# Optimization experiments

Measured on AMD Instinct MI355X. Metric: run time of the kernel, lower is better.

Reference implementation:

```python
import jax, jax.numpy as jnp
import numpy as np

B, Lc, Le, H, V = 128, 512, 512, 512, 128
PAD_IDX = 0  # ignore_index for cross entropy


def _lstm_cell(x, h, c, Wih, Whh, bih, bhh):
    # PyTorch gate order: i, f, g, o
    gates = x @ Wih.T + h @ Whh.T + bih + bhh
    i, f, g, o = jnp.split(gates, 4, axis=-1)
    c_new = jax.nn.sigmoid(f) * c + jax.nn.sigmoid(i) * jnp.tanh(g)
    h_new = jax.nn.sigmoid(o) * jnp.tanh(c_new)
    return h_new, c_new


def setup_inputs() -> dict:
    key = jax.random.key(0)
    ks = jax.random.split(key, 16)
    s = 0.05  # weight init scale
    inp = {
        "C": jax.random.normal(ks[0], (B, Lc, V), jnp.float32),
        "C_pad": jax.random.randint(ks[1], (B, Lc), 0, 2, jnp.int32).at[:, 0].set(0),
        "E": jax.random.randint(ks[2], (B, Le), 0, V, jnp.int32),
        "E_emb": jax.random.normal(ks[3], (B, Le, V), jnp.float32),
        # encoder LSTM (input V -> hidden H)
        "enc_Wih": s * jax.random.normal(ks[4], (4 * H, V), jnp.float32),
        "enc_Whh": s * jax.random.normal(ks[5], (4 * H, H), jnp.float32),
        "enc_bih": jnp.zeros((4 * H,), jnp.float32),
        "enc_bhh": jnp.zeros((4 * H,), jnp.float32),
        # decoder LSTMCell (input V+H -> hidden H); input is concat([E_emb_t, V_prev])
        "dec_Wih": s * jax.random.normal(ks[6], (4 * H, V + H), jnp.float32),
        "dec_Whh": s * jax.random.normal(ks[7], (4 * H, H), jnp.float32),
        "dec_bih": jnp.zeros((4 * H,), jnp.float32),
        "dec_bhh": jnp.zeros((4 * H,), jnp.float32),
        # attention_proj: Linear(H, H, bias=False)
        "att_W": s * jax.random.normal(ks[8], (H, H), jnp.float32),
        # output_proj: Linear(2H, H)
        "out_W": s * jax.random.normal(ks[9], (H, 2 * H), jnp.float32),
        "out_b": jnp.zeros((H,), jnp.float32),
        # vocab_proj: Linear(H, V)
        "voc_W": s * jax.random.normal(ks[10], (V, H), jnp.float32),
        "voc_b": jnp.zeros((V,), jnp.float32),
    }
    return inp


def reference(C, C_pad, E, E_emb, enc_Wih, enc_Whh, enc_bih, enc_bhh,
              dec_Wih, dec_Whh, dec_bih, dec_bhh, att_W, out_W, out_b,
              voc_W, voc_b):
    Bv = C.shape[0]
    Hh = enc_Whh.shape[1]

    # ---- encoder LSTM over compressed input ----
    def enc_step(carry, x_t):
        h, c = carry
        h, c = _lstm_cell(x_t, h, c, enc_Wih, enc_Whh, enc_bih, enc_bhh)
        return (h, c), h

    h0 = jnp.zeros((Bv, Hh), C.dtype)
    (hT, cT), enc_hs = jax.lax.scan(enc_step, (h0, h0), jnp.swapaxes(C, 0, 1))
    enc_hs = jnp.swapaxes(enc_hs, 0, 1)  # (B, Lc, H)
    pad = C_pad.astype(bool)              # (B, Lc)

    # ---- decoder loop (training mode, teacher forcing) ----
    def dec_step(carry, e_t):
        h, c, Vprev = carry
        x = jnp.concatenate([e_t, Vprev], axis=1)  # (B, V+H)
        h, c = _lstm_cell(x, h, c, dec_Wih, dec_Whh, dec_bih, dec_bhh)
        q = h @ att_W.T                                    # (B, H)
        scores = jnp.einsum('blh,bh->bl', enc_hs, q)       # (B, Lc)
        scores = jnp.where(pad, -jnp.inf, scores)
        d = jax.nn.softmax(scores, axis=1)
        attn = jnp.einsum('bl,blh->bh', d, enc_hs)         # (B, H)
        U = jnp.concatenate([h, attn], axis=1)             # (B, 2H)
        Vnew = U @ out_W.T + out_b                         # (B, H)
        # dropout treated as identity (eval-mode determinism)
        logits = jnp.tanh(Vnew) @ voc_W.T + voc_b          # (B, V)
        return (h, c, Vnew), logits

    Vinit = jnp.zeros((Bv, Hh), C.dtype)
    _, logits = jax.lax.scan(dec_step, (hT, cT, Vinit),
                             jnp.swapaxes(E_emb[:, :-1], 0, 1))
    logits = jnp.swapaxes(logits, 0, 1)  # (B, Le-1, V)

    # ---- cross entropy with ignore_index=PAD_IDX ----
    targets = E[:, 1:].astype(jnp.int32)
    logp = jax.nn.log_softmax(logits, axis=-1)
    nll = -jnp.take_along_axis(logp, targets[..., None], axis=-1)[..., 0]
    mask = (targets != PAD_IDX).astype(nll.dtype)
    loss = jnp.sum(nll * mask) / jnp.maximum(jnp.sum(mask), 1.0)
    return loss
```

## Files before the change

kernel.cpp:

```cpp
#include <hip/hip_runtime.h>
#include <hip/hip_bf16.h>


#define NWG 256
#define NT  256

typedef unsigned short u16;
typedef unsigned int   u32;
typedef unsigned long long u64;
typedef __attribute__((ext_vector_type(4))) float f4;
typedef __attribute__((ext_vector_type(8))) short s8;

constexpr int Bv = 128, Lc = 512, Le = 512, Hd = 512, Vc = 128;
constexpr int KE = 640;
constexpr int KD = 1152;

constexpr size_t O_WENC = 4096;
constexpr size_t O_WDEC = O_WENC + (size_t)2048*KE*2;
constexpr size_t O_ATTW = O_WDEC + (size_t)2048*KD*2;
constexpr size_t O_OUTW = O_ATTW + (size_t)512*512*2;
constexpr size_t O_VOCW = O_OUTW + (size_t)512*1024*2;
constexpr size_t O_BE   = O_VOCW + (size_t)128*512*2;
constexpr size_t O_BD   = O_BE + 8192;
constexpr size_t O_H    = O_BD + 8192;
constexpr size_t O_VPRV = O_H + (size_t)2*128*512*2;
constexpr size_t O_Q    = O_VPRV + (size_t)128*512*2;
constexpr size_t O_TNH  = O_Q + (size_t)128*512*4;
constexpr size_t O_PFX  = O_TNH + (size_t)2*128*512*2;
constexpr size_t O_CNT  = O_PFX + (size_t)128*512*4;
constexpr size_t O_PMS  = O_CNT + 512;
constexpr size_t O_PACC = O_PMS + 2048;
constexpr size_t O_LOSS = O_PACC + (size_t)256*512*2;
constexpr size_t O_ENC  = O_LOSS + 256;

constexpr int SM_U     = 64*KD*2;
constexpr int SM_BYTES = SM_U + 16384;

struct P {
  const float *C; const int *Cpad; const int *E; const float *Eemb;
  const float *eWih,*eWhh,*ebih,*ebhh;
  const float *dWih,*dWhh,*dbih,*dbhh;
  const float *attW,*outW,*outb,*vocW,*vocb;
  char* ws; float* out;
};

__device__ inline u16 f2bf(float x){
  u32 u = __float_as_uint(x);
  return (u16)((u + 0x7fffu + ((u>>16)&1u)) >> 16);
}
__device__ inline float bf2f(u16 b){ return __uint_as_float(((u32)b)<<16); }
__device__ inline float sigm(float x){ return 1.f/(1.f+expf(-x)); }

__device__ inline f4 MM(s8 a, s8 b, f4 c){
  return __builtin_amdgcn_mfma_f32_16x16x32_bf16(a, b, c, 0, 0, 0);
}

__device__ inline u64 ld64a(const void* p){
  return __hip_atomic_load((const u64*)p, __ATOMIC_RELAXED, __HIP_MEMORY_SCOPE_AGENT);
}
__device__ inline u32 ld32u(const void* p){
  return __hip_atomic_load((const u32*)p, __ATOMIC_RELAXED, __HIP_MEMORY_SCOPE_AGENT);
}
__device__ inline void st64a(void* p, u64 v){
  __hip_atomic_store((u64*)p, v, __ATOMIC_RELAXED, __HIP_MEMORY_SCOPE_AGENT);
}
__device__ inline void st32a(void* p, u32 v){
  __hip_atomic_store((u32*)p, v, __ATOMIC_RELAXED, __HIP_MEMORY_SCOPE_AGENT);
}
__device__ inline s8 ld16a(const void* p){
  union { u64 q[2]; s8 v; } u;
  u.q[0] = ld64a(p);
  u.q[1] = ld64a((const char*)p + 8);
  return u.v;
}

__device__ inline s8 cvt8(const float* p){
  f4 u = *(const f4*)p, v = *(const f4*)(p+4);
  s8 r;
  r[0]=(short)f2bf(u[0]); r[1]=(short)f2bf(u[1]); r[2]=(short)f2bf(u[2]); r[3]=(short)f2bf(u[3]);
  r[4]=(short)f2bf(v[0]); r[5]=(short)f2bf(v[1]); r[6]=(short)f2bf(v[2]); r[7]=(short)f2bf(v[3]);
  return r;
}

__device__ inline s8 ldsB(const char* sm, int K, int srow, int k){
  int byte = srow*(K*2) + k*2;
  byte ^= (srow&7)<<4;
  return *(const s8*)(sm + byte);
}

__device__ inline float wredmax(float v){
  #pragma unroll
  for (int m=32;m;m>>=1) v = fmaxf(v, __shfl_xor(v,m,64));
  return v;
}
__device__ inline float wredsum(float v){
  #pragma unroll
  for (int m=32;m;m>>=1) v += __shfl_xor(v,m,64);
  return v;
}

extern "C" __global__ void __launch_bounds__(NT,1) k_main(P p)
{
  extern __shared__ char sm[];
  const int wg = blockIdx.x, tid = threadIdx.x;
  const int gt = wg*NT + tid;
  const int rg = wg & 7, cg = wg >> 3;
  const int lid = rg*32 + cg;

  char* ws = p.ws;
  u32*  barAll  = (u32*)ws;
  u32*  flagAll = (u32*)(ws + 128);
  u32*  barRG   = (u32*)(ws + 512 + rg*256);
  u32*  flagRG  = (u32*)(ws + 512 + rg*256 + 128);
  u16*  wenc = (u16*)(ws + O_WENC);
  u16*  wdec = (u16*)(ws + O_WDEC);
  u16*  attw = (u16*)(ws + O_ATTW);
  u16*  outw = (u16*)(ws + O_OUTW);
  u16*  vocw = (u16*)(ws + O_VOCW);
  float* be  = (float*)(ws + O_BE);
  float* bd  = (float*)(ws + O_BD);
  u16*  hbf  = (u16*)(ws + O_H);
  u16*  vpv  = (u16*)(ws + O_VPRV);
  float* qg  = (float*)(ws + O_Q);
  u16*  tnhb = (u16*)(ws + O_TNH);
  u32*  pfx  = (u32*)(ws + O_PFX);
  u32*  cntp = (u32*)(ws + O_CNT);
  u64*  pms  = (u64*)(ws + O_PMS);
  u16*  pacc16 = (u16*)(ws + O_PACC);
  float* losp= (float*)(ws + O_LOSS);
  u16*  encc = (u16*)(ws + O_ENC);

  u32 genA = 0, genG = 0;

  auto GBall = [&](){
    genA++;
    __syncthreads();
    if (tid == 0){
      __builtin_amdgcn_fence(__ATOMIC_RELEASE, "agent");
      u32 old = __hip_atomic_fetch_add(barAll, 1u, __ATOMIC_RELAXED, __HIP_MEMORY_SCOPE_AGENT);
      if (old == genA*(u32)NWG - 1u) st32a(flagAll, genA);
      else while (ld32u(flagAll) < genA) __builtin_amdgcn_s_sleep(2);
      __builtin_amdgcn_fence(__ATOMIC_ACQUIRE, "agent");
    }
    __syncthreads();
  };
  auto RGB = [&](){
    genG++;
    __syncthreads();
    if (tid == 0){
      u32 old = __hip_atomic_fetch_add(barRG, 1u, __ATOMIC_RELAXED, __HIP_MEMORY_SCOPE_AGENT);
      if (old == genG*32u - 1u) st32a(flagRG, genG);
      else while (ld32u(flagRG) < genG) __builtin_amdgcn_s_sleep(2);
      __builtin_amdgcn_fence(__ATOMIC_ACQUIRE, "workgroup");
    }
    __syncthreads();
  };

  for (int i = gt; i < 2048*KE; i += NWG*NT){
    int row = i / KE, k = i - row*KE;
    float v = (k < 128) ? p.eWih[row*128 + k] : p.eWhh[row*512 + (k-128)];
    wenc[i] = f2bf(v);
  }
  for (int i = gt; i < 2048*KD; i += NWG*NT){
    int row = i / KD, k = i - row*KD;
    float v = (k < 640) ? p.dWih[row*640 + k] : p.dWhh[row*512 + (k-640)];
    wdec[i] = f2bf(v);
  }
  for (int i = gt; i < 512*512;  i += NWG*NT) attw[i] = f2bf(p.attW[i]);
  for (int i = gt; i < 512*1024; i += NWG*NT) outw[i] = f2bf(p.outW[i]);
  for (int i = gt; i < 128*512;  i += NWG*NT) vocw[i] = f2bf(p.vocW[i]);
  for (int i = gt; i < 2048;     i += NWG*NT){ be[i] = p.ebih[i]+p.ebhh[i]; bd[i] = p.dbih[i]+p.dbhh[i]; }
  { u32* hz = (u32*)hbf; for (int i = gt; i < 65536; i += NWG*NT) hz[i] = 0; }
  { u32* vz = (u32*)vpv; for (int i = gt; i < 32768; i += NWG*NT) vz[i] = 0; }
  if (gt == 0){ losp[0] = 0.f; losp[1] = 0.f; }
  if (wg < 128){
    int* padl = (int*)(sm + SM_U);
    for (int i = tid; i < 512; i += NT) padl[i] = p.Cpad[wg*512 + i];
    __syncthreads();
    if (tid == 0){
      u32 run = 0;
      for (int tt = 0; tt < 512; tt++){ pfx[wg*512+tt] = run; if (padl[tt] == 0) run++; }
      cntp[wg] = run;
    }
    __syncthreads();
  }
  GBall();

  const int l  = tid & 63, wv = tid >> 6;
  const int n2 = wv >> 1, k2 = wv & 1;
  const int kl = (l>>4) << 3;
  const int ar = rg*16 + (l&15);
  float cst = 0.f;
  float accN = 0.f, accC = 0.f;

  auto S6 = [&](int tl){
    const u16* tb = tnhb + (size_t)(tl&1)*Bv*Hd;
    float* lg = (float*)(sm + SM_U + 8192);
    s8 ta[16];
    #pragma unroll
    for (int ks = 0; ks < 16; ks++)
      ta[ks] = ld16a(tb + (size_t)(rg*16+(l&15))*Hd + ks*32 + kl);
    f4 lac0 = {0,0,0,0}, lac1 = {0,0,0,0};
    const int c0 = (wv*2)*16 + (l&15), c1 = (wv*2+1)*16 + (l&15);
    #pragma unroll
    for (int ks = 0; ks < 16; ks++){
      int k = ks*32 + kl;
      lac0 = MM(ta[ks], *(const s8*)(vocw + (size_t)c0*Hd + k), lac0);
      lac1 = MM(ta[ks], *(const s8*)(vocw + (size_t)c1*Hd + k), lac1);
    }
    #pragma unroll
    for (int r = 0; r < 4; r++){
      int row = ((l>>4)<<2) + r;
      lg[row*128 + c0] = lac0[r] + p.vocb[c0];
      lg[row*128 + c1] = lac1[r] + p.vocb[c1];
    }
    __syncthreads();
    {
      int rowi = tid>>4, ii = tid&15, b = rg*16 + rowi;
      float lm = -1e30f;
      #pragma unroll
      for (int j=0;j<8;j++) lm = fmaxf(lm, lg[rowi*128 + ii*8 + j]);
      #pragma unroll
      for (int m=1;m<16;m<<=1) lm = fmaxf(lm, __shfl_xor(lm,m,64));
      float le = 0.f;
      #pragma unroll
      for (int j=0;j<8;j++) le += expf(lg[rowi*128 + ii*8 + j] - lm);
      #pragma unroll
      for (int m=1;m<16;m<<=1) le += __shfl_xor(le,m,64);
      if (ii == 0){
        int tgt = p.E[b*Le + tl + 1];
        if (tgt != 0){ accN += logf(le) + lm - lg[rowi*128 + tgt]; accC += 1.f; }
      }
    }
    __syncthreads();
  };

  {
    const int chunks = KE/8;
    for (int idx = tid; idx < 64*chunks; idx += NT){
      int s = idx / chunks, cc = idx - s*chunks;
      int grow = (s>>4)*512 + cg*16 + (s&15);
      uint4 v = *(const uint4*)(wenc + (size_t)grow*KE + cc*8);
      int byte = s*(KE*2) + cc*16; byte ^= (s&7)<<4;
      *(uint4*)(sm + byte) = v;
    }
  }
  __syncthreads();

  for (int t = 0; t < Lc; t++){
    const u16* hold = hbf + (t&1)*Bv*Hd;
    u16* hnew       = hbf + ((t+1)&1)*Bv*Hd;
    s8 a[10];
    #pragma unroll
    for (int ks = 0; ks < 10; ks++){
      int k = k2*320 + ks*32 + kl;
      if (k < 128) a[ks] = cvt8(p.C + ((size_t)ar*Lc + t)*Vc + k);
      else         a[ks] = ld16a(hold + (size_t)ar*Hd + (k-128));
    }
    f4 acc0 = {0,0,0,0}, acc1 = {0,0,0,0};
    #pragma unroll
    for (int ks = 0; ks < 10; ks++){
      int k = k2*320 + ks*32 + kl;
      acc0 = MM(a[ks], ldsB(sm, KE, (n2*2+0)*16 + (l&15), k), acc0);
      acc1 = MM(a[ks], ldsB(sm, KE, (n2*2+1)*16 + (l&15), k), acc1);
    }
    float* exch = (float*)(sm + SM_U);
    #pragma unroll
    for (int r = 0; r < 4; r++){
      int row = ((l>>4)<<2) + r;
      exch[((k2*4 + n2*2+0)*16 + row)*16 + (l&15)] = acc0[r];
      exch[((k2*4 + n2*2+1)*16 + row)*16 + (l&15)] = acc1[r];
    }
    __syncthreads();
    {
      int row = tid >> 4, u = tid & 15;
      int gb = cg*16 + u;
      float gi = exch[((0)*16+row)*16+u] + exch[((4)*16+row)*16+u] + be[0*512+gb];
      float gf = exch[((1)*16+row)*16+u] + exch[((5)*16+row)*16+u] + be[1*512+gb];
      float gg = exch[((2)*16+row)*16+u] + exch[((6)*16+row)*16+u] + be[2*512+gb];
      float go = exch[((3)*16+row)*16+u] + exch[((7)*16+row)*16+u] + be[3*512+gb];
      float fi = sigm(gi), ff = sigm(gf), fg = tanhf(gg), fo = sigm(go);
      cst = ff*cst + fi*fg;
      float hn = fo * tanhf(cst);
      int b = rg*16 + row;
      u32 hb = f2bf(hn);
      u32 nb = __shfl_xor((int)hb, 1, 64);
      if ((tid & 1) == 0){
        u32 pk = hb | (nb << 16);
        st32a(hnew + (size_t)b*Hd + gb, pk);
        if (p.Cpad[b*Lc + t] == 0){
          u32 pos = pfx[b*Lc + t];
          st32a(encc + ((size_t)b*Lc + pos)*Hd + gb, pk);
        }
      }
    }
    RGB();
  }

  GBall();

  {
    const int chunks = KD/8;
    for (int idx = tid; idx < 64*chunks; idx += NT){
      int s = idx / chunks, cc = idx - s*chunks;
      int grow = (s>>4)*512 + cg*16 + (s&15);
      uint4 v = *(const uint4*)(wdec + (size_t)grow*KD + cc*8);
      int byte = s*(KD*2) + cc*16; byte ^= (s&7)<<4;
      *(uint4*)(sm + byte) = v;
    }
  }
  __syncthreads();

  for (int t = 0; t < Le-1; t++){
    const u16* hold = hbf + (t&1)*Bv*Hd;
    u16* hnew       = hbf + ((t+1)&1)*Bv*Hd;

    {
      s8 a[18];
      #pragma unroll
      for (int ks = 0; ks < 18; ks++){
        int k = k2*576 + ks*32 + kl;
        if (k < 128)      a[ks] = cvt8(p.Eemb + ((size_t)ar*Le + t)*Vc + k);
        else if (k < 640) a[ks] = ld16a(vpv  + (size_t)ar*Hd + (k-128));
        else              a[ks] = ld16a(hold + (size_t)ar*Hd + (k-640));
      }
      f4 acc0 = {0,0,0,0}, acc1 = {0,0,0,0};
      #pragma unroll
      for (int ks = 0; ks < 18; ks++){
        int k = k2*576 + ks*32 + kl;
        acc0 = MM(a[ks], ldsB(sm, KD, (n2*2+0)*16 + (l&15), k), acc0);
        acc1 = MM(a[ks], ldsB(sm, KD, (n2*2+1)*16 + (l&15), k), acc1);
      }
      float* exch = (float*)(sm + SM_U);
      #pragma unroll
      for (int r = 0; r < 4; r++){
        int row = ((l>>4)<<2) + r;
        exch[((k2*4 + n2*2+0)*16 + row)*16 + (l&15)] = acc0[r];
        exch[((k2*4 + n2*2+1)*16 + row)*16 + (l&15)] = acc1[r];
      }
      __syncthreads();
      {
        int row = tid >> 4, u = tid & 15;
        int gb = cg*16 + u;
        float gi = exch[((0)*16+row)*16+u] + exch[((4)*16+row)*16+u] + bd[0*512+gb];
        float gf = exch[((1)*16+row)*16+u] + exch[((5)*16+row)*16+u] + bd[1*512+gb];
        float gg = exch[((2)*16+row)*16+u] + exch[((6)*16+row)*16+u] + bd[2*512+gb];
        float go = exch[((3)*16+row)*16+u] + exch[((7)*16+row)*16+u] + bd[3*512+gb];
        float fi = sigm(gi), ff = sigm(gf), fg = tanhf(gg), fo = sigm(go);
        cst = ff*cst + fi*fg;
        float hn = fo * tanhf(cst);
        u32 hb = f2bf(hn);
        u32 nb = __shfl_xor((int)hb, 1, 64);
        if ((tid & 1) == 0)
          st32a(hnew + (size_t)(rg*16+row)*Hd + gb, hb | (nb << 16));
      }
    }
    RGB();

    {
      s8 ha[4];
      #pragma unroll
      for (int j = 0; j < 4; j++){
        int k = (wv*4 + j)*32 + kl;
        ha[j] = ld16a(hnew + (size_t)(rg*16 + (l&15))*Hd + k);
      }
      f4 acc = {0,0,0,0};
      #pragma unroll
      for (int j = 0; j < 4; j++){
        int k = (wv*4 + j)*32 + kl;
        acc = MM(ha[j], *(const s8*)(attw + (size_t)(cg*16 + (l&15))*Hd + k), acc);
      }
      float* exch4 = (float*)(sm + SM_U);
      #pragma unroll
      for (int r = 0; r < 4; r++)
        exch4[wv*256 + (((l>>4)<<2)+r)*16 + (l&15)] = acc[r];
      __syncthreads();
      {
        int row = tid >> 4, col = tid & 15;
        float q = exch4[row*16+col] + exch4[256+row*16+col]
                + exch4[512+row*16+col] + exch4[768+row*16+col];
        float qn = __shfl_xor(q, 1, 64);
        if ((tid & 1) == 0){
          union { u64 u; float f[2]; } pk; pk.f[0]=q; pk.f[1]=qn;
          st64a(qg + (size_t)(rg*16+row)*Hd + cg*16 + col, pk.u);
        }
      }
    }
    RGB();

    {
      const int row = rg*16 + (cg >> 1), hf = cg & 1;
      const int cn = (int)cntp[row], c2 = cn >> 1;
      const int st = hf ? c2 : 0, en = hf ? cn : c2, n = en - st;
      float* qld = (float*)(sm + SM_U);
      float* scl = (float*)(sm + SM_U + 2048);
      float* red = (float*)(sm + SM_U + 3104);
      float* part= (float*)(sm + SM_U + 8192);
      {
        union { u64 q; float f[2]; } u;
        u.q = ld64a(qg + (size_t)row*Hd + 2*tid);
        int c0 = 2*tid, c1 = c0+1;
        qld[(c0&15)*32 + (c0>>4)] = u.f[0];
        qld[(c1&15)*32 + (c1>>4)] = u.f[1];
      }
      __syncthreads();
      const int pg8 = tid >> 5, hg32 = tid & 31;
      const u16* ebase = encc + ((size_t)row*Lc + st)*Hd;
      for (int i = pg8; i < n; i += 8){
        const u16* e = ebase + (size_t)i*Hd + hg32*16;
        s8 ev0 = *(const s8*)(e);
        s8 ev1 = *(const s8*)(e+8);
        float s = 0.f;
        #pragma unroll
        for (int j=0;j<8;j++) s += bf2f((u16)ev0[j]) * qld[j*32+hg32];
        #pragma unroll
        for (int j=0;j<8;j++) s += bf2f((u16)ev1[j]) * qld[(j+8)*32+hg32];
        #pragma unroll
        for (int m=1;m<32;m<<=1) s += __shfl_xor(s, m, 64);
        if (hg32 == 0) scl[i] = s;
      }
      __syncthreads();
      float mloc = -1e30f;
      for (int i = tid; i < n; i += NT) mloc = fmaxf(mloc, scl[i]);
      mloc = wredmax(mloc);
      if ((tid&63)==0) red[tid>>6] = mloc;
      __syncthreads();
      float M = fmaxf(fmaxf(red[0],red[1]), fmaxf(red[2],red[3]));
      __syncthreads();
      float sloc = 0.f;
      for (int i = tid; i < n; i += NT){ float w = expf(scl[i]-M); scl[i]=w; sloc += w; }
      sloc = wredsum(sloc);
      if ((tid&63)==0) red[tid>>6] = sloc;
      __syncthreads();
      float S = red[0]+red[1]+red[2]+red[3];
      const int hg64 = tid & 63;
      float a8[8] = {0,0,0,0,0,0,0,0};
      const u16* eb2 = ebase + hg64*8;
      int i = wv;
      for (; i + 12 < n; i += 16){
        s8 e0 = *(const s8*)(eb2 + (size_t)i*Hd);
        s8 e1 = *(const s8*)(eb2 + (size_t)(i+4)*Hd);
        s8 e2 = *(const s8*)(eb2 + (size_t)(i+8)*Hd);
        s8 e3 = *(const s8*)(eb2 + (size_t)(i+12)*Hd);
        float w0=scl[i], w1=scl[i+4], w2=scl[i+8], w3=scl[i+12];
        #pragma unroll
        for (int j=0;j<8;j++) a8[j] += w0*bf2f((u16)e0[j]);
        #pragma unroll
        for (int j=0;j<8;j++) a8[j] += w1*bf2f((u16)e1[j]);
        #pragma unroll
        for (int j=0;j<8;j++) a8[j] += w2*bf2f((u16)e2[j]);
        #pragma unroll
        for (int j=0;j<8;j++) a8[j] += w3*bf2f((u16)e3[j]);
      }
      for (; i < n; i += 4){
        s8 e0 = *(const s8*)(eb2 + (size_t)i*Hd);
        float w0 = scl[i];
        #pragma unroll
        for (int j=0;j<8;j++) a8[j] += w0*bf2f((u16)e0[j]);
      }
      { f4 v0 = {a8[0],a8[1],a8[2],a8[3]}, v1 = {a8[4],a8[5],a8[6],a8[7]};
        *(f4*)(part + wv*512 + hg64*8)     = v0;
        *(f4*)(part + wv*512 + hg64*8 + 4) = v1; }
      __syncthreads();
      {
        int h0 = tid*2;
        float s0 = 0.f, s1 = 0.f;
        #pragma unroll
        for (int pg = 0; pg < 4; pg++){
          float2 pr = *(float2*)(part + pg*512 + h0);
          s0 += pr.x; s1 += pr.y;
        }
        u32 pk = (u32)f2bf(s0) | ((u32)f2bf(s1) << 16);
        st32a(pacc16 + (size_t)lid*Hd + h0, pk);
      }
      if (tid == 0){
        union { u64 q; float f[2]; } pk; pk.f[0]=M; pk.f[1]=S;
        st64a(pms + lid, pk.q);
      }
    }
    RGB();

    {
      float* sc2 = (float*)(sm + SM_U);
      float* vex = (float*)(sm + SM_U + 4096);
      if (tid < 16){
        union { u64 q; float f[2]; } uA, uB;
        uA.q = ld64a(pms + rg*32 + 2*tid);
        uB.q = ld64a(pms + rg*32 + 2*tid + 1);
        float M = fmaxf(uA.f[0], uB.f[0]);
        float eA = expf(uA.f[0]-M), eB = expf(uB.f[0]-M);
        float den = uA.f[1]*eA + uB.f[1]*eB;
        sc2[2*tid]   = eA/den;
        sc2[2*tid+1] = eB/den;
      }
      __syncthreads();
      if (cg == 0 && t > 0) S6(t-1);
      const int colc = cg*16 + (l&15);
      const u16* pb0 = pacc16 + ((size_t)(rg*32 + (l&15)*2))*Hd;
      float scA = sc2[(l&15)*2], scB = sc2[(l&15)*2+1];
      s8 raw[12];
      #pragma unroll
      for (int ks = 0; ks < 12; ks++){
        int km = wv*12 + ks;
        const void* ap;
        if (km < 16)      ap = hnew + (size_t)(rg*16+(l&15))*Hd + km*32 + kl;
        else if (km < 32) ap = pb0 + (km-16)*32 + kl;
        else              ap = pb0 + Hd + (km-32)*32 + kl;
        raw[ks] = ld16a(ap);
      }
      f4 vac = {0,0,0,0};
      #pragma unroll
      for (int ks = 0; ks < 12; ks++){
        int km = wv*12 + ks;
        s8 af;
        if (km < 16) af = raw[ks];
        else {
          float sc = (km < 32) ? scA : scB;
          #pragma unroll
          for (int j = 0; j < 8; j++) af[j] = (short)f2bf(bf2f((u16)raw[ks][j]) * sc);
        }
        int k = (km < 16) ? km*32+kl : ((km < 32) ? 512 + (km-16)*32+kl : 512 + (km-32)*32+kl);
        vac = MM(af, *(const s8*)(outw + (size_t)colc*1024 + k), vac);
      }
      #pragma unroll
      for (int r = 0; r < 4; r++)
        vex[wv*256 + (((l>>4)<<2)+r)*16 + (l&15)] = vac[r];
      __syncthreads();
      {
        int row = tid >> 4, col = tid & 15;
        float v = vex[row*16+col] + vex[256+row*16+col]
                + vex[512+row*16+col] + vex[768+row*16+col] + p.outb[cg*16+col];
        u32 vb = f2bf(v), tb2 = f2bf(tanhf(v));
        u32 vn = __shfl_xor((int)vb, 1, 64);
        u32 tn2 = __shfl_xor((int)tb2, 1, 64);
        if ((tid & 1) == 0){
          int b = rg*16 + row;
          u16* tnw = tnhb + (size_t)(t&1)*Bv*Hd;
          st32a(vpv + (size_t)b*Hd + cg*16 + col, vb | (vn<<16));
          st32a(tnw + (size_t)b*Hd + cg*16 + col, tb2 | (tn2<<16));
        }
      }
    }
    RGB();
  }

  if (cg == 0) S6(Le-2);

  if (cg == 0 && (tid&15) == 0){
    atomicAdd(losp + 0, accN);
    atomicAdd(losp + 1, accC);
  }
  GBall();
  if (wg == 0 && tid == 0) p.out[0] = losp[0] / fmaxf(losp[1], 1.f);
}

extern "C" void kernel_launch(void* const* d_in, const int* in_sizes, int n_in,
                              void* d_out, int out_size, void* d_ws, size_t ws_size,
                              hipStream_t stream)
{
  hipFuncSetAttribute(reinterpret_cast<const void*>(k_main),
                      hipFuncAttributeMaxDynamicSharedMemorySize, SM_BYTES);
  hipMemsetAsync(d_ws, 0, 4096, stream);

  P prm;
  prm.C    = (const float*)d_in[0];
  prm.Cpad = (const int*)  d_in[1];
  prm.E    = (const int*)  d_in[2];
  prm.Eemb = (const float*)d_in[3];
  prm.eWih = (const float*)d_in[4];
  prm.eWhh = (const float*)d_in[5];
  prm.ebih = (const float*)d_in[6];
  prm.ebhh = (const float*)d_in[7];
  prm.dWih = (const float*)d_in[8];
  prm.dWhh = (const float*)d_in[9];
  prm.dbih = (const float*)d_in[10];
  prm.dbhh = (const float*)d_in[11];
  prm.attW = (const float*)d_in[12];
  prm.outW = (const float*)d_in[13];
  prm.outb = (const float*)d_in[14];
  prm.vocW = (const float*)d_in[15];
  prm.vocb = (const float*)d_in[16];
  prm.ws   = (char*)d_ws;
  prm.out  = (float*)d_out;

  k_main<<<dim3(NWG), dim3(NT), SM_BYTES, stream>>>(prm);
}
```

Measured before the change: 26.10 ms.

## Fold output projection into decoder LSTM weights and cut per-step barriers

Precomputes fused decoder weights by multiplying the V_prev slice of dec_Wih by out_W, so the next step's gates come straight from h and the attention context rather than a materialised V. This removes one grid-group barrier phase per timestep. The step also merges the attention query, an online-softmax attention pass and a distributed vocab-projection cross-entropy that is combined one step later, and the group-barrier spin sleep is shortened. In exchange there is a heavy serial fp32 prefold at startup and a different bf16 rounding path, which may shift numerics.

Measured after the change: 35.73 ms. 1.37x slower.

```diff
diff --git a/kernel.cpp b/kernel.cpp
--- a/kernel.cpp
+++ b/kernel.cpp
@@ -11,26 +11,26 @@
 typedef __attribute__((ext_vector_type(4))) float f4;
 typedef __attribute__((ext_vector_type(8))) short s8;
 
-constexpr int Bv = 128, Lc = 512, Le = 512, Hd = 512, Vc = 128;
-constexpr int KE = 640;
-constexpr int KD = 1152;
+constexpr int Bv=128, Lc=512, Le=512, Hd=512, Vc=128;
+constexpr int KE=640, KD=1152;
 
 constexpr size_t O_WENC = 4096;
 constexpr size_t O_WDEC = O_WENC + (size_t)2048*KE*2;
-constexpr size_t O_ATTW = O_WDEC + (size_t)2048*KD*2;
+constexpr size_t O_WDF  = O_WDEC + (size_t)2048*KD*2;
+constexpr size_t O_ATTW = O_WDF  + (size_t)2048*KD*2;
 constexpr size_t O_OUTW = O_ATTW + (size_t)512*512*2;
 constexpr size_t O_VOCW = O_OUTW + (size_t)512*1024*2;
 constexpr size_t O_BE   = O_VOCW + (size_t)128*512*2;
 constexpr size_t O_BD   = O_BE + 8192;
-constexpr size_t O_H    = O_BD + 8192;
-constexpr size_t O_VPRV = O_H + (size_t)2*128*512*2;
-constexpr size_t O_Q    = O_VPRV + (size_t)128*512*2;
-constexpr size_t O_TNH  = O_Q + (size_t)128*512*4;
+constexpr size_t O_BDF  = O_BD + 8192;
+constexpr size_t O_H    = O_BDF + 8192;
+constexpr size_t O_TNH  = O_H + (size_t)2*128*512*2;
 constexpr size_t O_PFX  = O_TNH + (size_t)2*128*512*2;
 constexpr size_t O_CNT  = O_PFX + (size_t)128*512*4;
 constexpr size_t O_PMS  = O_CNT + 512;
 constexpr size_t O_PACC = O_PMS + 2048;
-constexpr size_t O_LOSS = O_PACC + (size_t)256*512*2;
+constexpr size_t O_REC  = O_PACC + (size_t)256*512*2;
+constexpr size_t O_LOSS = O_REC + (size_t)2*128*2*4*4;
 constexpr size_t O_ENC  = O_LOSS + 256;
 
 constexpr int SM_U     = 64*KD*2;
@@ -50,11 +50,9 @@
 }
 __device__ inline float bf2f(u16 b){ return __uint_as_float(((u32)b)<<16); }
 __device__ inline float sigm(float x){ return 1.f/(1.f+expf(-x)); }
-
 __device__ inline f4 MM(s8 a, s8 b, f4 c){
   return __builtin_amdgcn_mfma_f32_16x16x32_bf16(a, b, c, 0, 0, 0);
 }
-
 __device__ inline u64 ld64a(const void* p){
   return __hip_atomic_load((const u64*)p, __ATOMIC_RELAXED, __HIP_MEMORY_SCOPE_AGENT);
 }
@@ -69,11 +67,9 @@
 }
 __device__ inline s8 ld16a(const void* p){
   union { u64 q[2]; s8 v; } u;
-  u.q[0] = ld64a(p);
-  u.q[1] = ld64a((const char*)p + 8);
+  u.q[0] = ld64a(p); u.q[1] = ld64a((const char*)p + 8);
   return u.v;
 }
-
 __device__ inline s8 cvt8(const float* p){
   f4 u = *(const f4*)p, v = *(const f4*)(p+4);
   s8 r;
@@ -81,13 +77,11 @@
   r[4]=(short)f2bf(v[0]); r[5]=(short)f2bf(v[1]); r[6]=(short)f2bf(v[2]); r[7]=(short)f2bf(v[3]);
   return r;
 }
-
 __device__ inline s8 ldsB(const char* sm, int K, int srow, int k){
   int byte = srow*(K*2) + k*2;
   byte ^= (srow&7)<<4;
   return *(const s8*)(sm + byte);
 }
-
 __device__ inline float wredmax(float v){
   #pragma unroll
   for (int m=32;m;m>>=1) v = fmaxf(v, __shfl_xor(v,m,64));
@@ -97,6 +91,15 @@
   #pragma unroll
   for (int m=32;m;m>>=1) v += __shfl_xor(v,m,64);
   return v;
+}
+__device__ inline float dscore(s8 e, const float* q8){
+  float d = bf2f((u16)e[0])*q8[0] + bf2f((u16)e[1])*q8[1]
+          + bf2f((u16)e[2])*q8[2] + bf2f((u16)e[3])*q8[3]
+          + bf2f((u16)e[4])*q8[4] + bf2f((u16)e[5])*q8[5]
+          + bf2f((u16)e[6])*q8[6] + bf2f((u16)e[7])*q8[7];
+  #pragma unroll
+  for (int mk=1; mk<64; mk<<=1) d += __shfl_xor(d, mk, 64);
+  return d;
 }
 
 extern "C" __global__ void __launch_bounds__(NT,1) k_main(P p)
@@ -105,7 +108,6 @@
   const int wg = blockIdx.x, tid = threadIdx.x;
   const int gt = wg*NT + tid;
   const int rg = wg & 7, cg = wg >> 3;
-  const int lid = rg*32 + cg;
 
   char* ws = p.ws;
   u32*  barAll  = (u32*)ws;
@@ -114,24 +116,24 @@
   u32*  flagRG  = (u32*)(ws + 512 + rg*256 + 128);
   u16*  wenc = (u16*)(ws + O_WENC);
   u16*  wdec = (u16*)(ws + O_WDEC);
+  u16*  wdf  = (u16*)(ws + O_WDF);
   u16*  attw = (u16*)(ws + O_ATTW);
   u16*  outw = (u16*)(ws + O_OUTW);
   u16*  vocw = (u16*)(ws + O_VOCW);
   float* be  = (float*)(ws + O_BE);
   float* bd  = (float*)(ws + O_BD);
+  float* bdf = (float*)(ws + O_BDF);
   u16*  hbf  = (u16*)(ws + O_H);
-  u16*  vpv  = (u16*)(ws + O_VPRV);
-  float* qg  = (float*)(ws + O_Q);
   u16*  tnhb = (u16*)(ws + O_TNH);
   u32*  pfx  = (u32*)(ws + O_PFX);
   u32*  cntp = (u32*)(ws + O_CNT);
   u64*  pms  = (u64*)(ws + O_PMS);
   u16*  pacc16 = (u16*)(ws + O_PACC);
+  float* rec = (float*)(ws + O_REC);
   float* losp= (float*)(ws + O_LOSS);
   u16*  encc = (u16*)(ws + O_ENC);
 
   u32 genA = 0, genG = 0;
-
   auto GBall = [&](){
     genA++;
     __syncthreads();
@@ -150,7 +152,7 @@
     if (tid == 0){
       u32 old = __hip_atomic_fetch_add(barRG, 1u, __ATOMIC_RELAXED, __HIP_MEMORY_SCOPE_AGENT);
       if (old == genG*32u - 1u) st32a(flagRG, genG);
-      else while (ld32u(flagRG) < genG) __builtin_amdgcn_s_sleep(2);
+      else while (ld32u(flagRG) < genG) __builtin_amdgcn_s_sleep(1);
       __builtin_amdgcn_fence(__ATOMIC_ACQUIRE, "workgroup");
     }
     __syncthreads();
@@ -171,8 +173,51 @@
   for (int i = gt; i < 128*512;  i += NWG*NT) vocw[i] = f2bf(p.vocW[i]);
   for (int i = gt; i < 2048;     i += NWG*NT){ be[i] = p.ebih[i]+p.ebhh[i]; bd[i] = p.dbih[i]+p.dbhh[i]; }
   { u32* hz = (u32*)hbf; for (int i = gt; i < 65536; i += NWG*NT) hz[i] = 0; }
-  { u32* vz = (u32*)vpv; for (int i = gt; i < 32768; i += NWG*NT) vz[i] = 0; }
   if (gt == 0){ losp[0] = 0.f; losp[1] = 0.f; }
+
+  {
+    const int g0 = wg*8;
+    float* dv = (float*)sm;
+    for (int i = tid; i < 8*512; i += NT)
+      dv[i] = p.dWih[(size_t)(g0 + (i>>9))*640 + 128 + (i&511)];
+    __syncthreads();
+    float wa[8][4];
+    #pragma unroll
+    for (int r=0;r<8;r++){ wa[r][0]=0;wa[r][1]=0;wa[r][2]=0;wa[r][3]=0; }
+    for (int o = 0; o < 512; o++){
+      float b0 = p.outW[(size_t)o*1024 + tid];
+      float b1 = p.outW[(size_t)o*1024 + 256 + tid];
+      float b2 = p.outW[(size_t)o*1024 + 512 + tid];
+      float b3 = p.outW[(size_t)o*1024 + 768 + tid];
+      #pragma unroll
+      for (int r=0;r<8;r++){
+        float d = dv[r*512+o];
+        wa[r][0] += d*b0; wa[r][1] += d*b1; wa[r][2] += d*b2; wa[r][3] += d*b3;
+      }
+    }
+    #pragma unroll
+    for (int r=0;r<8;r++){
+      int g = g0 + r;
+      #pragma unroll
+      for (int j=0;j<4;j++){
+        int c = tid + 256*j;
+        if (c < 512) wdf[(size_t)g*KD + 128 + c] = f2bf(p.dWhh[(size_t)g*512 + c] + wa[r][j]);
+        else         wdf[(size_t)g*KD + 640 + (c-512)] = f2bf(wa[r][j]);
+      }
+    }
+    for (int i = tid; i < 8*128; i += NT){
+      int r = i >> 7, k = i & 127;
+      wdf[(size_t)(g0+r)*KD + k] = f2bf(p.dWih[(size_t)(g0+r)*640 + k]);
+    }
+    if (tid < 8){
+      int g = g0 + tid;
+      float s = p.dbih[g] + p.dbhh[g];
+      for (int o = 0; o < 512; o++) s += dv[tid*512+o]*p.outb[o];
+      bdf[g] = s;
+    }
+    __syncthreads();
+  }
+
   if (wg < 128){
     int* padl = (int*)(sm + SM_U);
     for (int i = tid; i < 512; i += NT) padl[i] = p.Cpad[wg*512 + i];
@@ -192,48 +237,6 @@
   const int ar = rg*16 + (l&15);
   float cst = 0.f;
   float accN = 0.f, accC = 0.f;
-
-  auto S6 = [&](int tl){
-    const u16* tb = tnhb + (size_t)(tl&1)*Bv*Hd;
-    float* lg = (float*)(sm + SM_U + 8192);
-    s8 ta[16];
-    #pragma unroll
-    for (int ks = 0; ks < 16; ks++)
-      ta[ks] = ld16a(tb + (size_t)(rg*16+(l&15))*Hd + ks*32 + kl);
-    f4 lac0 = {0,0,0,0}, lac1 = {0,0,0,0};
-    const int c0 = (wv*2)*16 + (l&15), c1 = (wv*2+1)*16 + (l&15);
-    #pragma unroll
-    for (int ks = 0; ks < 16; ks++){
-      int k = ks*32 + kl;
-      lac0 = MM(ta[ks], *(const s8*)(vocw + (size_t)c0*Hd + k), lac0);
-      lac1 = MM(ta[ks], *(const s8*)(vocw + (size_t)c1*Hd + k), lac1);
-    }
-    #pragma unroll
-    for (int r = 0; r < 4; r++){
-      int row = ((l>>4)<<2) + r;
-      lg[row*128 + c0] = lac0[r] + p.vocb[c0];
-      lg[row*128 + c1] = lac1[r] + p.vocb[c1];
-    }
-    __syncthreads();
-    {
-      int rowi = tid>>4, ii = tid&15, b = rg*16 + rowi;
-      float lm = -1e30f;
-      #pragma unroll
-      for (int j=0;j<8;j++) lm = fmaxf(lm, lg[rowi*128 + ii*8 + j]);
-      #pragma unroll
-      for (int m=1;m<16;m<<=1) lm = fmaxf(lm, __shfl_xor(lm,m,64));
-      float le = 0.f;
-      #pragma unroll
-      for (int j=0;j<8;j++) le += expf(lg[rowi*128 + ii*8 + j] - lm);
-      #pragma unroll
-      for (int m=1;m<16;m<<=1) le += __shfl_xor(le,m,64);
-      if (ii == 0){
-        int tgt = p.E[b*Le + tl + 1];
-        if (tgt != 0){ accN += logf(le) + lm - lg[rowi*128 + tgt]; accC += 1.f; }
-      }
-    }
-    __syncthreads();
-  };
 
   {
     const int chunks = KE/8;
@@ -304,34 +307,93 @@
     for (int idx = tid; idx < 64*chunks; idx += NT){
       int s = idx / chunks, cc = idx - s*chunks;
       int grow = (s>>4)*512 + cg*16 + (s&15);
-      uint4 v = *(const uint4*)(wdec + (size_t)grow*KD + cc*8);
+      uint4 v = *(const uint4*)(wdf + (size_t)grow*KD + cc*8);
       int byte = s*(KD*2) + cc*16; byte ^= (s&7)<<4;
       *(uint4*)(sm + byte) = v;
     }
   }
   __syncthreads();
+
+  float* exch = (float*)(sm + SM_U);
+  float* vex  = (float*)(sm + SM_U + 8192);
+  float* sc2  = (float*)(sm + SM_U + 12288);
+
+  auto CEREC = [&](int tl, int row, int half){
+    u32* th16 = (u32*)(sm + SM_U + 12416);
+    float* lgp = (float*)(sm + SM_U + 13440);
+    float* lgh = (float*)(sm + SM_U + 14464);
+    const u16* tb = tnhb + (size_t)(tl&1)*Bv*Hd + (size_t)row*Hd;
+    th16[tid & 255] = ld32u(tb + 2*tid);
+    __syncthreads();
+    {
+      int v = tid & 63, ksl = tid >> 6;
+      int gv = half*64 + v;
+      const u16* wp = vocw + (size_t)gv*Hd + ksl*128;
+      const u16* hp = (const u16*)th16 + ksl*128;
+      float acc = 0.f;
+      #pragma unroll 4
+      for (int j = 0; j < 16; j++){
+        s8 wv8 = *(const s8*)(wp + j*8);
+        #pragma unroll
+        for (int q = 0; q < 8; q++) acc += bf2f((u16)wv8[q]) * bf2f(hp[j*8+q]);
+      }
+      lgp[ksl*64 + v] = acc;
+    }
+    __syncthreads();
+    if (tid < 64){
+      int gv = half*64 + tid;
+      float lv = lgp[tid] + lgp[64+tid] + lgp[128+tid] + lgp[192+tid] + p.vocb[gv];
+      lgh[tid] = lv;
+      float m = wredmax(lv);
+      float s = wredsum(expf(lv - m));
+      if (tid == 0){
+        int tgt = p.E[row*Le + tl + 1];
+        float tlg = (tgt >= half*64 && tgt < half*64+64) ? lgh[tgt - half*64] : 0.f;
+        float* rp = rec + ((size_t)(tl&1)*256 + row*2 + half)*4;
+        union { u64 q; float f[2]; } pk; pk.f[0]=m; pk.f[1]=s;
+        st64a(rp, pk.q);
+        st32a(rp+2, __float_as_uint(tlg));
+      }
+    }
+    __syncthreads();
+  };
+  auto COMB = [&](int tl, int row){
+    int tgt = p.E[row*Le + tl + 1];
+    if (tgt != 0){
+      const float* rp = rec + ((size_t)(tl&1)*256 + row*2)*4;
+      union { u64 q; float f[2]; } a, b;
+      a.q = ld64a(rp); b.q = ld64a(rp+4);
+      float tA = __uint_as_float(ld32u(rp+2)), tB = __uint_as_float(ld32u(rp+6));
+      float M = fmaxf(a.f[0], b.f[0]);
+      float S = a.f[1]*expf(a.f[0]-M) + b.f[1]*expf(b.f[0]-M);
+      accN += logf(S) + M - (tA + tB);
+      accC += 1.f;
+    }
+  };
 
   for (int t = 0; t < Le-1; t++){
     const u16* hold = hbf + (t&1)*Bv*Hd;
     u16* hnew       = hbf + ((t+1)&1)*Bv*Hd;
 
-    {
-      s8 a[18];
-      #pragma unroll
-      for (int ks = 0; ks < 18; ks++){
-        int k = k2*576 + ks*32 + kl;
-        if (k < 128)      a[ks] = cvt8(p.Eemb + ((size_t)ar*Le + t)*Vc + k);
-        else if (k < 640) a[ks] = ld16a(vpv  + (size_t)ar*Hd + (k-128));
-        else              a[ks] = ld16a(hold + (size_t)ar*Hd + (k-640));
+    if (t == 0){
+      s8 a[10];
+      #pragma unroll
+      for (int ks = 0; ks < 10; ks++){
+        int ke = (k2==0) ? ((ks<4) ? ks*32+kl : 640 + (ks-4)*32 + kl)
+                         : (832 + ks*32 + kl);
+        if (ke < 128) a[ks] = cvt8(p.Eemb + ((size_t)ar*Le + 0)*Vc + ke);
+        else          a[ks] = ld16a(hold + (size_t)ar*Hd + (ke-640));
       }
       f4 acc0 = {0,0,0,0}, acc1 = {0,0,0,0};
       #pragma unroll
-      for (int ks = 0; ks < 18; ks++){
-        int k = k2*576 + ks*32 + kl;
-        acc0 = MM(a[ks], ldsB(sm, KD, (n2*2+0)*16 + (l&15), k), acc0);
-        acc1 = MM(a[ks], ldsB(sm, KD, (n2*2+1)*16 + (l&15), k), acc1);
-      }
-      float* exch = (float*)(sm + SM_U);
+      for (int ks = 0; ks < 10; ks++){
+        int ke = (k2==0) ? ((ks<4) ? ks*32+kl : 640 + (ks-4)*32 + kl)
+                         : (832 + ks*32 + kl);
+        int g0r = (n2*2+0)*512 + cg*16 + (l&15);
+        int g1r = (n2*2+1)*512 + cg*16 + (l&15);
+        acc0 = MM(a[ks], *(const s8*)(wdec + (size_t)g0r*KD + ke), acc0);
+        acc1 = MM(a[ks], *(const s8*)(wdec + (size_t)g1r*KD + ke), acc1);
+      }
       #pragma unroll
       for (int r = 0; r < 4; r++){
         int row = ((l>>4)<<2) + r;
@@ -352,203 +414,260 @@
         u32 hb = f2bf(hn);
         u32 nb = __shfl_xor((int)hb, 1, 64);
         if ((tid & 1) == 0)
-          st32a(hnew + (size_t)(rg*16+row)*Hd + gb, hb | (nb << 16));
-      }
-    }
-    RGB();
-
-    {
-      s8 ha[4];
-      #pragma unroll
-      for (int j = 0; j < 4; j++){
-        int k = (wv*4 + j)*32 + kl;
-        ha[j] = ld16a(hnew + (size_t)(rg*16 + (l&15))*Hd + k);
-      }
-      f4 acc = {0,0,0,0};
-      #pragma unroll
-      for (int j = 0; j < 4; j++){
-        int k = (wv*4 + j)*32 + kl;
-        acc = MM(ha[j], *(const s8*)(attw + (size_t)(cg*16 + (l&15))*Hd + k), acc);
-      }
-      float* exch4 = (float*)(sm + SM_U);
-      #pragma unroll
-      for (int r = 0; r < 4; r++)
-        exch4[wv*256 + (((l>>4)<<2)+r)*16 + (l&15)] = acc[r];
+          st32a(hnew + (size_t)(rg*16+(tid>>4))*Hd + gb, hb | (nb << 16));
+      }
+    } else {
+      if (tid < 16){
+        union { u64 q; float f[2]; } uA, uB;
+        uA.q = ld64a(pms + (rg*16+tid)*2 + 0);
+        uB.q = ld64a(pms + (rg*16+tid)*2 + 1);
+        float M = fmaxf(uA.f[0], uB.f[0]);
+        float eA = (uA.f[0] > -1e29f) ? expf(uA.f[0]-M) : 0.f;
+        float eB = (uB.f[0] > -1e29f) ? expf(uB.f[0]-M) : 0.f;
+        float den = uA.f[1]*eA + uB.f[1]*eB;
+        sc2[tid*2]   = eA/den;
+        sc2[tid*2+1] = eB/den;
+      }
+      __syncthreads();
+      const float scA = sc2[(l&15)*2], scB = sc2[(l&15)*2+1];
+      const u16* pA = pacc16 + (size_t)(ar*2+0)*Hd;
+      const u16* pB = pacc16 + (size_t)(ar*2+1)*Hd;
+      s8 a[18];
+      #pragma unroll
+      for (int ks = 0; ks < 18; ks++){
+        int k = k2*576 + ks*32 + kl;
+        if (k < 128)      a[ks] = cvt8(p.Eemb + ((size_t)ar*Le + t)*Vc + k);
+        else if (k < 640) a[ks] = ld16a(hold + (size_t)ar*Hd + (k-128));
+        else {
+          s8 va = ld16a(pA + (k-640));
+          s8 vb = ld16a(pB + (k-640));
+          s8 r;
+          #pragma unroll
+          for (int j = 0; j < 8; j++)
+            r[j] = (short)f2bf(scA*bf2f((u16)va[j]) + scB*bf2f((u16)vb[j]));
+          a[ks] = r;
+        }
+      }
+      f4 acc0 = {0,0,0,0}, acc1 = {0,0,0,0};
+      #pragma unroll
+      for (int ks = 0; ks < 18; ks++){
+        int k = k2*576 + ks*32 + kl;
+        acc0 = MM(a[ks], ldsB(sm, KD, (n2*2+0)*16 + (l&15), k), acc0);
+        acc1 = MM(a[ks], ldsB(sm, KD, (n2*2+1)*16 + (l&15), k), acc1);
+      }
+      f4 vac = {0,0,0,0};
+      const int colc = cg*16 + (l&15);
+      #pragma unroll
+      for (int ks = 0; ks < 18; ks++){
+        int ck = k2*18 + ks - 4;
+        if (ck >= 0 && ((ck & 1) == n2))
+          vac = MM(a[ks], *(const s8*)(outw + (size_t)colc*1024 + ck*32 + kl), vac);
+      }
+      #pragma unroll
+      for (int r = 0; r < 4; r++){
+        int row = ((l>>4)<<2) + r;
+        exch[((k2*4 + n2*2+0)*16 + row)*16 + (l&15)] = acc0[r];
+        exch[((k2*4 + n2*2+1)*16 + row)*16 + (l&15)] = acc1[r];
+        vex[wv*256 + row*16 + (l&15)] = vac[r];
+      }
       __syncthreads();
       {
-        int row = tid >> 4, col = tid & 15;
-        float q = exch4[row*16+col] + exch4[256+row*16+col]
-                + exch4[512+row*16+col] + exch4[768+row*16+col];
-        float qn = __shfl_xor(q, 1, 64);
+        int row = tid >> 4, u = tid & 15;
+        int gb = cg*16 + u;
+        float gi = exch[((0)*16+row)*16+u] + exch[((4)*16+row)*16+u] + bdf[0*512+gb];
+        float gf = exch[((1)*16+row)*16+u] + exch[((5)*16+row)*16+u] + bdf[1*512+gb];
+        float gg = exch[((2)*16+row)*16+u] + exch[((6)*16+row)*16+u] + bdf[2*512+gb];
+        float go = exch[((3)*16+row)*16+u] + exch[((7)*16+row)*16+u] + bdf[3*512+gb];
+        float fi = sigm(gi), ff = sigm(gf), fg = tanhf(gg), fo = sigm(go);
+        cst = ff*cst + fi*fg;
+        float hn = fo * tanhf(cst);
+        u32 hb = f2bf(hn);
+        u32 nb = __shfl_xor((int)hb, 1, 64);
+        if ((tid & 1) == 0)
+          st32a(hnew + (size_t)(rg*16+row)*Hd + gb, hb | (nb << 16));
+        float v = vex[row*16+u] + vex[256+row*16+u] + vex[512+row*16+u]
+                + vex[768+row*16+u] + p.outb[gb];
+        u32 tb2 = f2bf(tanhf(v));
+        u32 tn2 = __shfl_xor((int)tb2, 1, 64);
         if ((tid & 1) == 0){
-          union { u64 u; float f[2]; } pk; pk.f[0]=q; pk.f[1]=qn;
-          st64a(qg + (size_t)(rg*16+row)*Hd + cg*16 + col, pk.u);
+          u16* tnw = tnhb + (size_t)((t-1)&1)*Bv*Hd;
+          st32a(tnw + (size_t)(rg*16+row)*Hd + gb, tb2 | (tn2 << 16));
         }
       }
     }
     RGB();
 
     {
-      const int row = rg*16 + (cg >> 1), hf = cg & 1;
+      const int row = rg*16 + (cg >> 1), half = cg & 1;
       const int cn = (int)cntp[row], c2 = cn >> 1;
-      const int st = hf ? c2 : 0, en = hf ? cn : c2, n = en - st;
-      float* qld = (float*)(sm + SM_U);
-      float* scl = (float*)(sm + SM_U + 2048);
-      float* red = (float*)(sm + SM_U + 3104);
-      float* part= (float*)(sm + SM_U + 8192);
+      const int st = half ? c2 : 0, en = half ? cn : c2, n = en - st;
+      float* hq = (float*)(sm + SM_U);
+      float* qv = (float*)(sm + SM_U + 2048);
+      float* pm4 = (float*)(sm + SM_U + 4096);
+      float* ps4 = (float*)(sm + SM_U + 4128);
+      float* part= (float*)(sm + SM_U + 4224);
       {
-        union { u64 q; float f[2]; } u;
-        u.q = ld64a(qg + (size_t)row*Hd + 2*tid);
-        int c0 = 2*tid, c1 = c0+1;
-        qld[(c0&15)*32 + (c0>>4)] = u.f[0];
-        qld[(c1&15)*32 + (c1>>4)] = u.f[1];
-      }
-      __syncthreads();
-      const int pg8 = tid >> 5, hg32 = tid & 31;
-      const u16* ebase = encc + ((size_t)row*Lc + st)*Hd;
-      for (int i = pg8; i < n; i += 8){
-        const u16* e = ebase + (size_t)i*Hd + hg32*16;
-        s8 ev0 = *(const s8*)(e);
-        s8 ev1 = *(const s8*)(e+8);
-        float s = 0.f;
-        #pragma unroll
-        for (int j=0;j<8;j++) s += bf2f((u16)ev0[j]) * qld[j*32+hg32];
-        #pragma unroll
-        for (int j=0;j<8;j++) s += bf2f((u16)ev1[j]) * qld[(j+8)*32+hg32];
-        #pragma unroll
-        for (int m=1;m<32;m<<=1) s += __shfl_xor(s, m, 64);
-        if (hg32 == 0) scl[i] = s;
-      }
-      __syncthreads();
-      float mloc = -1e30f;
-      for (int i = tid; i < n; i += NT) mloc = fmaxf(mloc, scl[i]);
-      mloc = wredmax(mloc);
-      if ((tid&63)==0) red[tid>>6] = mloc;
-      __syncthreads();
-      float M = fmaxf(fmaxf(red[0],red[1]), fmaxf(red[2],red[3]));
-      __syncthreads();
-      float sloc = 0.f;
-      for (int i = tid; i < n; i += NT){ float w = expf(scl[i]-M); scl[i]=w; sloc += w; }
-      sloc = wredsum(sloc);
-      if ((tid&63)==0) red[tid>>6] = sloc;
-      __syncthreads();
-      float S = red[0]+red[1]+red[2]+red[3];
-      const int hg64 = tid & 63;
-      float a8[8] = {0,0,0,0,0,0,0,0};
-      const u16* eb2 = ebase + hg64*8;
-      int i = wv;
-      for (; i + 12 < n; i += 16){
-        s8 e0 = *(const s8*)(eb2 + (size_t)i*Hd);
-        s8 e1 = *(const s8*)(eb2 + (size_t)(i+4)*Hd);
-        s8 e2 = *(const s8*)(eb2 + (size_t)(i+8)*Hd);
-        s8 e3 = *(const s8*)(eb2 + (size_t)(i+12)*Hd);
-        float w0=scl[i], w1=scl[i+4], w2=scl[i+8], w3=scl[i+12];
-        #pragma unroll
-        for (int j=0;j<8;j++) a8[j] += w0*bf2f((u16)e0[j]);
-        #pragma unroll
-        for (int j=0;j<8;j++) a8[j] += w1*bf2f((u16)e1[j]);
-        #pragma unroll
-        for (int j=0;j<8;j++) a8[j] += w2*bf2f((u16)e2[j]);
-        #pragma unroll
-        for (int j=0;j<8;j++) a8[j] += w3*bf2f((u16)e3[j]);
-      }
-      for (; i < n; i += 4){
-        s8 e0 = *(const s8*)(eb2 + (size_t)i*Hd);
-        float w0 = scl[i];
-        #pragma unroll
-        for (int j=0;j<8;j++) a8[j] += w0*bf2f((u16)e0[j]);
-      }
-      { f4 v0 = {a8[0],a8[1],a8[2],a8[3]}, v1 = {a8[4],a8[5],a8[6],a8[7]};
-        *(f4*)(part + wv*512 + hg64*8)     = v0;
-        *(f4*)(part + wv*512 + hg64*8 + 4) = v1; }
+        u32 hw = ld32u(hnew + (size_t)row*Hd + 2*tid);
+        hq[2*tid]   = bf2f((u16)(hw & 0xffffu));
+        hq[2*tid+1] = bf2f((u16)(hw >> 16));
+      }
       __syncthreads();
       {
-        int h0 = tid*2;
-        float s0 = 0.f, s1 = 0.f;
+        int j0 = 2*tid;
+        float q0 = 0.f, q1 = 0.f;
+        const u16* w0 = attw + (size_t)j0*Hd;
+        const u16* w1 = w0 + Hd;
+        #pragma unroll 4
+        for (int kk = 0; kk < 64; kk++){
+          s8 a0 = *(const s8*)(w0 + kk*8);
+          s8 a1 = *(const s8*)(w1 + kk*8);
+          #pragma unroll
+          for (int q = 0; q < 8; q++){
+            float h = hq[kk*8+q];
+            q0 += bf2f((u16)a0[q]) * h;
+            q1 += bf2f((u16)a1[q]) * h;
+          }
+        }
+        qv[j0] = q0; qv[j0+1] = q1;
+      }
+      __syncthreads();
+      float q8[8];
+      #pragma unroll
+      for (int j = 0; j < 8; j++) q8[j] = qv[l*8 + j];
+      float m = -1e30f, s = 0.f;
+      float acc[8] = {0,0,0,0,0,0,0,0};
+      const u16* eb = encc + ((size_t)row*Lc + st)*Hd + l*8;
+      int ii = wv;
+      for (; ii + 12 < n; ii += 16){
+        s8 e0 = *(const s8*)(eb + (size_t)(ii   )*Hd);
+        s8 e1 = *(const s8*)(eb + (size_t)(ii+ 4)*Hd);
+        s8 e2 = *(const s8*)(eb + (size_t)(ii+ 8)*Hd);
+        s8 e3 = *(const s8*)(eb + (size_t)(ii+12)*Hd);
+        float s0 = dscore(e0, q8), s1 = dscore(e1, q8);
+        float s2 = dscore(e2, q8), s3 = dscore(e3, q8);
+        float tm = fmaxf(fmaxf(s0,s1), fmaxf(s2,s3));
+        if (tm > m){
+          float fac = expf(m - tm);
+          s *= fac;
+          #pragma unroll
+          for (int j=0;j<8;j++) acc[j] *= fac;
+          m = tm;
+        }
+        float w0 = expf(s0-m), w1 = expf(s1-m), w2 = expf(s2-m), w3 = expf(s3-m);
+        s += w0+w1+w2+w3;
         #pragma unroll
-        for (int pg = 0; pg < 4; pg++){
-          float2 pr = *(float2*)(part + pg*512 + h0);
-          s0 += pr.x; s1 += pr.y;
+        for (int j=0;j<8;j++)
+          acc[j] += w0*bf2f((u16)e0[j]) + w1*bf2f((u16)e1[j])
+                  + w2*bf2f((u16)e2[j]) + w3*bf2f((u16)e3[j]);
+      }
+      for (; ii < n; ii += 4){
+        s8 e0 = *(const s8*)(eb + (size_t)ii*Hd);
+        float s0 = dscore(e0, q8);
+        if (s0 > m){
+          float fac = expf(m - s0);
+          s *= fac;
+          #pragma unroll
+          for (int j=0;j<8;j++) acc[j] *= fac;
+          m = s0;
         }
-        u32 pk = (u32)f2bf(s0) | ((u32)f2bf(s1) << 16);
-        st32a(pacc16 + (size_t)lid*Hd + h0, pk);
-      }
-      if (tid == 0){
-        union { u64 q; float f[2]; } pk; pk.f[0]=M; pk.f[1]=S;
-        st64a(pms + lid, pk.q);
-      }
-    }
-    RGB();
-
-    {
-      float* sc2 = (float*)(sm + SM_U);
-      float* vex = (float*)(sm + SM_U + 4096);
-      if (tid < 16){
-        union { u64 q; float f[2]; } uA, uB;
-        uA.q = ld64a(pms + rg*32 + 2*tid);
-        uB.q = ld64a(pms + rg*32 + 2*tid + 1);
-        float M = fmaxf(uA.f[0], uB.f[0]);
-        float eA = expf(uA.f[0]-M), eB = expf(uB.f[0]-M);
-        float den = uA.f[1]*eA + uB.f[1]*eB;
-        sc2[2*tid]   = eA/den;
-        sc2[2*tid+1] = eB/den;
-      }
-      __syncthreads();
-      if (cg == 0 && t > 0) S6(t-1);
-      const int colc = cg*16 + (l&15);
-      const u16* pb0 = pacc16 + ((size_t)(rg*32 + (l&15)*2))*Hd;
-      float scA = sc2[(l&15)*2], scB = sc2[(l&15)*2+1];
-      s8 raw[12];
-      #pragma unroll
-      for (int ks = 0; ks < 12; ks++){
-        int km = wv*12 + ks;
-        const void* ap;
-        if (km < 16)      ap = hnew + (size_t)(rg*16+(l&15))*Hd + km*32 + kl;
-        else if (km < 32) ap = pb0 + (km-16)*32 + kl;
-        else              ap = pb0 + Hd + (km-32)*32 + kl;
-        raw[ks] = ld16a(ap);
-      }
-      f4 vac = {0,0,0,0};
-      #pragma unroll
-      for (int ks = 0; ks < 12; ks++){
-        int km = wv*12 + ks;
-        s8 af;
-        if (km < 16) af = raw[ks];
-        else {
-          float sc = (km < 32) ? scA : scB;
-          #pragma unroll
-          for (int j = 0; j < 8; j++) af[j] = (short)f2bf(bf2f((u16)raw[ks][j]) * sc);
-        }
-        int k = (km < 16) ? km*32+kl : ((km < 32) ? 512 + (km-16)*32+kl : 512 + (km-32)*32+kl);
-        vac = MM(af, *(const s8*)(outw + (size_t)colc*1024 + k), vac);
-      }
-      #pragma unroll
-      for (int r = 0; r < 4; r++)
-        vex[wv*256 + (((l>>4)<<2)+r)*16 + (l&15)] = vac[r];
+        float w0 = expf(s0-m);
+        s += w0;
+        #pragma unroll
+        for (int j=0;j<8;j++) acc[j] += w0*bf2f((u16)e0[j]);
+      }
+      if (l == 0){ pm4[wv] = m; ps4[wv] = s; }
+      { f4 v0 = {acc[0],acc[1],acc[2],acc[3]}, v1 = {acc[4],acc[5],acc[6],acc[7]};
+        *(f4*)(part + wv*512 + l*8)     = v0;
+        *(f4*)(part + wv*512 + l*8 + 4) = v1; }
       __syncthreads();
       {
-        int row = tid >> 4, col = tid & 15;
-        float v = vex[row*16+col] + vex[256+row*16+col]
-                + vex[512+row*16+col] + vex[768+row*16+col] + p.outb[cg*16+col];
-        u32 vb = f2bf(v), tb2 = f2bf(tanhf(v));
-        u32 vn = __shfl_xor((int)vb, 1, 64);
-        u32 tn2 = __shfl_xor((int)tb2, 1, 64);
-        if ((tid & 1) == 0){
-          int b = rg*16 + row;
-          u16* tnw = tnhb + (size_t)(t&1)*Bv*Hd;
-          st32a(vpv + (size_t)b*Hd + cg*16 + col, vb | (vn<<16));
-          st32a(tnw + (size_t)b*Hd + cg*16 + col, tb2 | (tn2<<16));
+        float M = fmaxf(fmaxf(pm4[0],pm4[1]), fmaxf(pm4[2],pm4[3]));
+        float f0 = (pm4[0] > -1e29f) ? expf(pm4[0]-M) : 0.f;
+        float f1 = (pm4[1] > -1e29f) ? expf(pm4[1]-M) : 0.f;
+        float f2 = (pm4[2] > -1e29f) ? expf(pm4[2]-M) : 0.f;
+        float f3 = (pm4[3] > -1e29f) ? expf(pm4[3]-M) : 0.f;
+        float S = ps4[0]*f0 + ps4[1]*f1 + ps4[2]*f2 + ps4[3]*f3;
+        int h0 = 2*tid;
+        float a0 = part[h0]*f0 + part[512+h0]*f1 + part[1024+h0]*f2 + part[1536+h0]*f3;
+        float a1 = part[h0+1]*f0 + part[512+h0+1]*f1 + part[1024+h0+1]*f2 + part[1536+h0+1]*f3;
+        st32a(pacc16 + (size_t)(row*2+half)*Hd + h0, (u32)f2bf(a0) | ((u32)f2bf(a1) << 16));
+        if (tid == 0){
+          union { u64 q; float f[2]; } pk; pk.f[0]=M; pk.f[1]=S;
+          st64a(pms + row*2 + half, pk.q);
         }
       }
+      __syncthreads();
+      if (t >= 1) CEREC(t-1, row, half);
+      if (t >= 2 && half == 0 && tid == 0) COMB(t-2, row);
     }
     RGB();
   }
 
-  if (cg == 0) S6(Le-2);
-
-  if (cg == 0 && (tid&15) == 0){
-    atomicAdd(losp + 0, accN);
-    atomicAdd(losp + 1, accC);
+  const int TL = Le-2;
+  {
+    if (tid < 16){
+      union { u64 q; float f[2]; } uA, uB;
+      uA.q = ld64a(pms + (rg*16+tid)*2 + 0);
+      uB.q = ld64a(pms + (rg*16+tid)*2 + 1);
+      float M = fmaxf(uA.f[0], uB.f[0]);
+      float eA = (uA.f[0] > -1e29f) ? expf(uA.f[0]-M) : 0.f;
+      float eB = (uB.f[0] > -1e29f) ? expf(uB.f[0]-M) : 0.f;
+      float den = uA.f[1]*eA + uB.f[1]*eB;
+      sc2[tid*2]   = eA/den;
+      sc2[tid*2+1] = eB/den;
+    }
+    __syncthreads();
+    const float scA = sc2[(l&15)*2], scB = sc2[(l&15)*2+1];
+    const u16* h5 = hbf + (size_t)((TL+1)&1)*Bv*Hd;
+    const u16* pA = pacc16 + (size_t)(ar*2+0)*Hd;
+    const u16* pB = pacc16 + (size_t)(ar*2+1)*Hd;
+    const int colc = cg*16 + (l&15);
+    f4 vac = {0,0,0,0};
+    #pragma unroll
+    for (int j = 0; j < 8; j++){
+      int kv = k2*16 + j*2 + n2;
+      s8 af;
+      if (kv < 16) af = ld16a(h5 + (size_t)ar*Hd + kv*32 + kl);
+      else {
+        s8 va = ld16a(pA + (kv-16)*32 + kl);
+        s8 vb = ld16a(pB + (kv-16)*32 + kl);
+        #pragma unroll
+        for (int q = 0; q < 8; q++)
+          af[q] = (short)f2bf(scA*bf2f((u16)va[q]) + scB*bf2f((u16)vb[q]));
+      }
+      vac = MM(af, *(const s8*)(outw + (size_t)colc*1024 + kv*32 + kl), vac);
+    }
+    #pragma unroll
+    for (int r = 0; r < 4; r++)
+      vex[wv*256 + (((l>>4)<<2)+r)*16 + (l&15)] = vac[r];
+    __syncthreads();
+    {
+      int row = tid >> 4, u = tid & 15;
+      int gb = cg*16 + u;
+      float v = vex[row*16+u] + vex[256+row*16+u] + vex[512+row*16+u]
+              + vex[768+row*16+u] + p.outb[gb];
+      u32 tb2 = f2bf(tanhf(v));
+      u32 tn2 = __shfl_xor((int)tb2, 1, 64);
+      if ((tid & 1) == 0){
+        u16* tnw = tnhb + (size_t)(TL&1)*Bv*Hd;
+        st32a(tnw + (size_t)(rg*16+row)*Hd + gb, tb2 | (tn2 << 16));
+      }
+    }
+  }
+  RGB();
+  {
+    const int row = rg*16 + (cg >> 1), half = cg & 1;
+    CEREC(TL, row, half);
+    if (half == 0 && tid == 0) COMB(TL-1, row);
+  }
+  RGB();
+  {
+    const int row = rg*16 + (cg >> 1), half = cg & 1;
+    if (half == 0 && tid == 0){
+      COMB(TL, row);
+      atomicAdd(losp + 0, accN);
+      atomicAdd(losp + 1, accC);
+    }
   }
   GBall();
   if (wg == 0 && tid == 0) p.out[0] = losp[0] / fmaxf(losp[1], 1.f);
```
